# Kernel tuning notes

Hardware: AMD Instinct MI355X
Metric: run time of the kernel (lower is better)

Reference implementation:

```python
import jax, jax.numpy as jnp
import numpy as np

# Phi-3-small blocksparse config
S = 2048            # num prompt tokens (single sequence)
H = 32              # num query heads
HKV = 8             # num kv heads (GQA)
D = 128             # head size
BLK = 64            # sparse_block_size
LOCAL = 16          # local_blocks
VERT = 8            # vert_stride
SCALE = 0.08838834764831845  # 1/sqrt(128)
HEAD_SLIDE = max(1, VERT // H)  # = 1 (per-head vertical offset, homo_head=False)


def _blocksparse_mask():
    """Per-head local+strided block-sparse causal mask, shape [H, S, S] bool."""
    nb = S // BLK
    qb = jnp.arange(nb)[None, :, None]   # query block idx
    kb = jnp.arange(nb)[None, None, :]   # key block idx
    h = jnp.arange(H)[:, None, None]
    blk = (qb >= kb) & (
        (qb - kb < LOCAL) | (((kb + h * HEAD_SLIDE + 1) % VERT) == 0)
    )  # [H, nb, nb]
    dense = jnp.repeat(jnp.repeat(blk, BLK, axis=1), BLK, axis=2)  # [H, S, S]
    causal = jnp.arange(S)[:, None] >= jnp.arange(S)[None, :]
    return dense & causal[None]


def setup_inputs() -> dict:
    key = jax.random.key(0)
    k1, k2, k3 = jax.random.split(key, 3)
    return {
        "query": jax.random.normal(k1, (S, H * D), dtype=jnp.float32),
        "key": jax.random.normal(k2, (S, HKV * D), dtype=jnp.float32),
        "value": jax.random.normal(k3, (S, HKV * D), dtype=jnp.float32),
    }


def reference(query, key, value):
    q = query.reshape(S, H, D)
    k = jnp.repeat(key.reshape(S, HKV, D), H // HKV, axis=1)    # GQA expand
    v = jnp.repeat(value.reshape(S, HKV, D), H // HKV, axis=1)
    scores = jnp.einsum("qhd,khd->hqk", q, k) * SCALE           # [H, S, S]
    mask = _blocksparse_mask()
    scores = jnp.where(mask, scores, jnp.finfo(scores.dtype).min)
    p = jax.nn.softmax(scores, axis=-1)
    out = jnp.einsum("hqk,khd->qhd", p, v)                      # [S, H, D]
    return out.reshape(S, H * D)
```

## Files before the change

### kernel.cpp

```cpp
#include <hip/hip_runtime.h>


typedef __bf16 bf16_t;
typedef __bf16 bf16x4 __attribute__((ext_vector_type(4)));
typedef __bf16 bf16x8 __attribute__((ext_vector_type(8)));
typedef float  fx4    __attribute__((ext_vector_type(4)));
typedef unsigned u32x2 __attribute__((ext_vector_type(2)));
typedef unsigned u32x4 __attribute__((ext_vector_type(4)));

#define SL2E_F 0.1275240614354876f

__device__ inline void load_lds16(const bf16_t* g, bf16_t* l) {
    __builtin_amdgcn_global_load_lds(
        (const __attribute__((address_space(1))) void*)g,
        (__attribute__((address_space(3))) void*)l, 16, 0, 0);
}

__device__ inline unsigned cvt_pk_bf16(float lo, float hi) {
    unsigned r;
    asm("v_cvt_pk_bf16_f32 %0, %1, %2" : "=v"(r) : "v"(lo), "v"(hi));
    return r;
}

__device__ inline u32x2 quad_gather(unsigned A) {
    u32x2 bc = __builtin_amdgcn_permlane32_swap(A, A, false, false);
    return __builtin_amdgcn_permlane16_swap(bc[0], bc[1], false, false);
}

__global__ void prep_kernel(const float* __restrict__ K, const float* __restrict__ V,
                            bf16_t* __restrict__ Kb, bf16_t* __restrict__ VT)
{
    const int blk = blockIdx.x;
    {
        const size_t base = (size_t)blk * 4096 + (size_t)threadIdx.x * 16;
        fx4 a0 = *(const fx4*)(K + base);
        fx4 a1 = *(const fx4*)(K + base + 4);
        fx4 a2 = *(const fx4*)(K + base + 8);
        fx4 a3 = *(const fx4*)(K + base + 12);
        bf16x8 f0, f1;
        f0[0]=(bf16_t)a0[0]; f0[1]=(bf16_t)a0[1]; f0[2]=(bf16_t)a0[2]; f0[3]=(bf16_t)a0[3];
        f0[4]=(bf16_t)a1[0]; f0[5]=(bf16_t)a1[1]; f0[6]=(bf16_t)a1[2]; f0[7]=(bf16_t)a1[3];
        f1[0]=(bf16_t)a2[0]; f1[1]=(bf16_t)a2[1]; f1[2]=(bf16_t)a2[2]; f1[3]=(bf16_t)a2[3];
        f1[4]=(bf16_t)a3[0]; f1[5]=(bf16_t)a3[1]; f1[6]=(bf16_t)a3[2]; f1[7]=(bf16_t)a3[3];
        *(bf16x8*)(Kb + base)     = f0;
        *(bf16x8*)(Kb + base + 8) = f1;
    }
    __shared__ __align__(16) bf16_t T[64 * 72];
    const int s0 = (blk & 31) * 64;
    const int c0 = (blk >> 5) * 64;
    const int tx = threadIdx.x & 15, ty = threadIdx.x >> 4;
    fx4 a0 = *(const fx4*)(V + (size_t)(s0 + ty * 4 + 0) * 1024 + c0 + tx * 4);
    fx4 a1 = *(const fx4*)(V + (size_t)(s0 + ty * 4 + 1) * 1024 + c0 + tx * 4);
    fx4 a2 = *(const fx4*)(V + (size_t)(s0 + ty * 4 + 2) * 1024 + c0 + tx * 4);
    fx4 a3 = *(const fx4*)(V + (size_t)(s0 + ty * 4 + 3) * 1024 + c0 + tx * 4);
#pragma unroll
    for (int j = 0; j < 4; ++j) {
        bf16x4 f = { (bf16_t)a0[j], (bf16_t)a1[j], (bf16_t)a2[j], (bf16_t)a3[j] };
        *(bf16x4*)&T[(tx * 4 + j) * 72 + ty * 4] = f;
    }
    __syncthreads();
    const int c = threadIdx.x >> 2, part = threadIdx.x & 3;
    bf16x8 x0 = *(const bf16x8*)&T[c * 72 + part * 16];
    bf16x8 x1 = *(const bf16x8*)&T[c * 72 + part * 16 + 8];
    bf16_t* dst = VT + (size_t)(c0 + c) * 2048 + s0 + part * 16;
    *(bf16x8*)(dst)     = x0;
    *(bf16x8*)(dst + 8) = x1;
}

__launch_bounds__(128, 1)
__global__ void bsfa_kernel(const float* __restrict__ Q,
                            const bf16_t* __restrict__ Kb,
                            const bf16_t* __restrict__ VT,
                            float* __restrict__ O)
{
    const int blk  = blockIdx.x;
    const int kvh  = blk & 7;
    const int h    = kvh * 4 + ((blk >> 3) & 3);
    const int qb   = 31 - (blk >> 5);
    const int tid  = threadIdx.x;
    const int rh   = tid >> 6;
    const int lane = tid & 63;
    const int l15  = lane & 15;
    const int quad = lane >> 4;
    const bool hi32 = (lane >= 32);

    __shared__ __align__(16) bf16_t Ks[2][64 * 128];
    __shared__ __align__(16) bf16_t Vs[2][128 * 64];

    const int row0 = qb * 64 + rh * 32;

    const bf16_t* kg = Kb + (size_t)kvh * 128;
    const bf16_t* vg = VT + ((size_t)kvh * 128) * 2048;

    bf16x8 qf[2][4];
#pragma unroll
    for (int qt = 0; qt < 2; ++qt) {
        const float* qp = Q + (size_t)(row0 + qt * 16 + l15) * 4096 + h * 128;
#pragma unroll
        for (int kc = 0; kc < 4; ++kc) {
            fx4 a = *(const fx4*)(qp + kc * 32 + quad * 8);
            fx4 b = *(const fx4*)(qp + kc * 32 + quad * 8 + 4);
            bf16x8 f;
            f[0] = (bf16_t)(a[0] * SL2E_F); f[1] = (bf16_t)(a[1] * SL2E_F);
            f[2] = (bf16_t)(a[2] * SL2E_F); f[3] = (bf16_t)(a[3] * SL2E_F);
            f[4] = (bf16_t)(b[0] * SL2E_F); f[5] = (bf16_t)(b[1] * SL2E_F);
            f[6] = (bf16_t)(b[2] * SL2E_F); f[7] = (bf16_t)(b[3] * SL2E_F);
            qf[qt][kc] = f;
        }
    }

    bf16x8 ones;
#pragma unroll
    for (int i = 0; i < 8; ++i) ones[i] = (bf16_t)1.0f;

    fx4 oacc[8][2];
    fx4 lacc[2];
    const fx4 zero4 = {0.0f, 0.0f, 0.0f, 0.0f};
#pragma unroll
    for (int dt = 0; dt < 8; ++dt)
#pragma unroll
        for (int qt = 0; qt < 2; ++qt) oacc[dt][qt] = zero4;
    lacc[0] = zero4; lacc[1] = zero4;

    auto stage = [&](int kb, int bi) {
        const bf16_t* kt_g = kg + ((size_t)kb << 16);
        const bf16_t* vt_g = vg + ((size_t)kb << 6);
        bf16_t* kd = &Ks[bi][0];
        bf16_t* vd = &Vs[bi][0];
#pragma unroll
        for (int i = 0; i < 8; ++i) {
            const int chunk = i * 128 + tid;
            const int krow = chunk >> 4;
            const int kc   = (chunk & 15) ^ (krow & 15);
            load_lds16(kt_g + (size_t)krow * 1024 + kc * 8, kd + (size_t)chunk * 8);
            const int vrow = chunk >> 3;
            const int vc   = (chunk & 7) ^ (vrow & 7);
            load_lds16(vt_g + (size_t)vrow * 2048 + vc * 8, vd + (size_t)chunk * 8);
        }
    };

    const int loc0 = (qb > 15) ? (qb - 15) : 0;
    const int kb0s = (8 - ((h + 1) & 7)) & 7;
    auto nxt = [&](int kb) -> int {
        if (kb < loc0) { const int t = kb + 8; return (t <= qb - 16) ? t : loc0; }
        return (kb < qb) ? (kb + 1) : -1;
    };

    int kb = (qb - 16 >= kb0s) ? kb0s : loc0;
    stage(kb, 0);
    __syncthreads();

    int cur = 0;
    while (kb >= 0) {
        const int nkb = nxt(kb);
        if (nkb >= 0) stage(nkb, cur ^ 1);

        const bf16_t* kd = &Ks[cur][0];
        const bf16_t* vd = &Vs[cur][0];

        fx4 sacc[4][2];
#pragma unroll
        for (int kt = 0; kt < 4; ++kt)
#pragma unroll
            for (int qt = 0; qt < 2; ++qt) sacc[kt][qt] = zero4;
#pragma unroll
        for (int kc = 0; kc < 4; ++kc)
#pragma unroll
            for (int kt = 0; kt < 4; ++kt) {
                bf16x8 kf = *(const bf16x8*)&kd[(kt * 16 + l15) * 128 + ((kc * 4 + quad) ^ l15) * 8];
#pragma unroll
                for (int qt = 0; qt < 2; ++qt)
                    sacc[kt][qt] = __builtin_amdgcn_mfma_f32_16x16x32_bf16(
                        kf, qf[qt][kc], sacc[kt][qt], 0, 0, 0);
            }

        if (kb == qb) {
#pragma unroll
            for (int kt = 0; kt < 4; ++kt)
#pragma unroll
                for (int qt = 0; qt < 2; ++qt)
#pragma unroll
                    for (int r = 0; r < 4; ++r) {
                        const int k_in = kt * 16 + quad * 4 + r;
                        const int q_in = rh * 32 + qt * 16 + l15;
                        if (q_in < k_in) sacc[kt][qt][r] = -1e30f;
                    }
        }

#pragma unroll
        for (int kt = 0; kt < 4; ++kt)
#pragma unroll
            for (int qt = 0; qt < 2; ++qt)
#pragma unroll
                for (int r = 0; r < 4; ++r)
                    sacc[kt][qt][r] = exp2f(sacc[kt][qt][r]);

        bf16x8 pf[2][2];
#pragma unroll
        for (int qt = 0; qt < 2; ++qt)
#pragma unroll
            for (int kcg = 0; kcg < 2; ++kcg) {
                const unsigned a00 = cvt_pk_bf16(sacc[2*kcg  ][qt][0], sacc[2*kcg  ][qt][1]);
                const unsigned a01 = cvt_pk_bf16(sacc[2*kcg  ][qt][2], sacc[2*kcg  ][qt][3]);
                const unsigned a10 = cvt_pk_bf16(sacc[2*kcg+1][qt][0], sacc[2*kcg+1][qt][1]);
                const unsigned a11 = cvt_pk_bf16(sacc[2*kcg+1][qt][2], sacc[2*kcg+1][qt][3]);
                const u32x2 g00 = quad_gather(a00);
                const u32x2 g01 = quad_gather(a01);
                const u32x2 g10 = quad_gather(a10);
                const u32x2 g11 = quad_gather(a11);
                u32x4 pw;
                pw[0] = hi32 ? g10[0] : g00[0];
                pw[1] = hi32 ? g11[0] : g01[0];
                pw[2] = hi32 ? g10[1] : g00[1];
                pw[3] = hi32 ? g11[1] : g01[1];
                pf[qt][kcg] = __builtin_bit_cast(bf16x8, pw);
            }

#pragma unroll
        for (int kcg = 0; kcg < 2; ++kcg) {
#pragma unroll
            for (int dt = 0; dt < 8; ++dt) {
                bf16x8 vf = *(const bf16x8*)&vd[(dt * 16 + l15) * 64 + ((kcg * 4 + quad) ^ (l15 & 7)) * 8];
#pragma unroll
                for (int qt = 0; qt < 2; ++qt)
                    oacc[dt][qt] = __builtin_amdgcn_mfma_f32_16x16x32_bf16(
                        vf, pf[qt][kcg], oacc[dt][qt], 0, 0, 0);
            }
#pragma unroll
            for (int qt = 0; qt < 2; ++qt)
                lacc[qt] = __builtin_amdgcn_mfma_f32_16x16x32_bf16(
                    ones, pf[qt][kcg], lacc[qt], 0, 0, 0);
        }

        __syncthreads();
        kb = nkb; cur ^= 1;
    }

#pragma unroll
    for (int qt = 0; qt < 2; ++qt) {
        const float inv = 1.0f / lacc[qt][0];
#pragma unroll
        for (int dt = 0; dt < 8; ++dt) {
            fx4 o = oacc[dt][qt] * inv;
            *(fx4*)(O + (size_t)(row0 + qt * 16 + l15) * 4096 + h * 128 + dt * 16 + quad * 4) = o;
        }
    }
}

extern "C" void kernel_launch(void* const* d_in, const int* in_sizes, int n_in,
                              void* d_out, int out_size, void* d_ws, size_t ws_size,
                              hipStream_t stream) {
    (void)in_sizes; (void)n_in; (void)ws_size; (void)out_size;
    const float* q = (const float*)d_in[0];
    const float* k = (const float*)d_in[1];
    const float* v = (const float*)d_in[2];
    float* o = (float*)d_out;

    bf16_t* Kb = (bf16_t*)d_ws;
    bf16_t* VT = Kb + (size_t)2048 * 1024;

    prep_kernel<<<dim3(512), dim3(256), 0, stream>>>(k, v, Kb, VT);
    bsfa_kernel<<<dim3(1024), dim3(128), 0, stream>>>(q, Kb, VT, o);
}
```

Before: 164.6 us.

## Load V fragments directly from global memory into registers, drop V LDS staging

V tiles are no longer staged in shared memory through async global-to-LDS copies. Each lane now loads its V MFMA fragments straight from global memory into registers, issued early and spread around the QK^T MFMAs to hide latency. This halves LDS use, and launch bounds are raised to allow two blocks per CU. The cost is higher register pressure (16 extra bf16x8 per lane), uncoalesced-ish strided global loads of V, and redundant V reads by the two waves of a block.

```diff
diff --git a/kernel.cpp b/kernel.cpp
--- a/kernel.cpp
+++ b/kernel.cpp
@@ -67,7 +67,7 @@
     *(bf16x8*)(dst + 8) = x1;
 }
 
-__launch_bounds__(128, 1)
+__launch_bounds__(128, 2)
 __global__ void bsfa_kernel(const float* __restrict__ Q,
                             const bf16_t* __restrict__ Kb,
                             const bf16_t* __restrict__ VT,
@@ -85,12 +85,11 @@
     const bool hi32 = (lane >= 32);
 
     __shared__ __align__(16) bf16_t Ks[2][64 * 128];
-    __shared__ __align__(16) bf16_t Vs[2][128 * 64];
 
     const int row0 = qb * 64 + rh * 32;
 
     const bf16_t* kg = Kb + (size_t)kvh * 128;
-    const bf16_t* vg = VT + ((size_t)kvh * 128) * 2048;
+    const bf16_t* vbase = VT + ((size_t)kvh * 128 + l15) * 2048 + quad * 8;
 
     bf16x8 qf[2][4];
 #pragma unroll
@@ -124,18 +123,13 @@
 
     auto stage = [&](int kb, int bi) {
         const bf16_t* kt_g = kg + ((size_t)kb << 16);
-        const bf16_t* vt_g = vg + ((size_t)kb << 6);
         bf16_t* kd = &Ks[bi][0];
-        bf16_t* vd = &Vs[bi][0];
 #pragma unroll
         for (int i = 0; i < 8; ++i) {
             const int chunk = i * 128 + tid;
             const int krow = chunk >> 4;
             const int kc   = (chunk & 15) ^ (krow & 15);
             load_lds16(kt_g + (size_t)krow * 1024 + kc * 8, kd + (size_t)chunk * 8);
-            const int vrow = chunk >> 3;
-            const int vc   = (chunk & 7) ^ (vrow & 7);
-            load_lds16(vt_g + (size_t)vrow * 2048 + vc * 8, vd + (size_t)chunk * 8);
         }
     };
 
@@ -156,7 +150,12 @@
         if (nkb >= 0) stage(nkb, cur ^ 1);
 
         const bf16_t* kd = &Ks[cur][0];
-        const bf16_t* vd = &Vs[cur][0];
+        const bf16_t* vp = vbase + ((size_t)kb << 6);
+
+        bf16x8 vfr0[8];
+#pragma unroll
+        for (int dt = 0; dt < 8; ++dt)
+            vfr0[dt] = *(const bf16x8*)(vp + (size_t)(dt * 16) * 2048);
 
         fx4 sacc[4][2];
 #pragma unroll
@@ -173,6 +172,11 @@
                     sacc[kt][qt] = __builtin_amdgcn_mfma_f32_16x16x32_bf16(
                         kf, qf[qt][kc], sacc[kt][qt], 0, 0, 0);
             }
+
+        bf16x8 vfr1[8];
+#pragma unroll
+        for (int dt = 0; dt < 8; ++dt)
+            vfr1[dt] = *(const bf16x8*)(vp + (size_t)(dt * 16) * 2048 + 32);
 
         if (kb == qb) {
 #pragma unroll
@@ -217,20 +221,25 @@
             }
 
 #pragma unroll
-        for (int kcg = 0; kcg < 2; ++kcg) {
-#pragma unroll
-            for (int dt = 0; dt < 8; ++dt) {
-                bf16x8 vf = *(const bf16x8*)&vd[(dt * 16 + l15) * 64 + ((kcg * 4 + quad) ^ (l15 & 7)) * 8];
-#pragma unroll
-                for (int qt = 0; qt < 2; ++qt)
-                    oacc[dt][qt] = __builtin_amdgcn_mfma_f32_16x16x32_bf16(
-                        vf, pf[qt][kcg], oacc[dt][qt], 0, 0, 0);
-            }
+        for (int dt = 0; dt < 8; ++dt)
 #pragma unroll
             for (int qt = 0; qt < 2; ++qt)
-                lacc[qt] = __builtin_amdgcn_mfma_f32_16x16x32_bf16(
-                    ones, pf[qt][kcg], lacc[qt], 0, 0, 0);
-        }
+                oacc[dt][qt] = __builtin_amdgcn_mfma_f32_16x16x32_bf16(
+                    vfr0[dt], pf[qt][0], oacc[dt][qt], 0, 0, 0);
+#pragma unroll
+        for (int qt = 0; qt < 2; ++qt)
+            lacc[qt] = __builtin_amdgcn_mfma_f32_16x16x32_bf16(
+                ones, pf[qt][0], lacc[qt], 0, 0, 0);
+#pragma unroll
+        for (int dt = 0; dt < 8; ++dt)
+#pragma unroll
+            for (int qt = 0; qt < 2; ++qt)
+                oacc[dt][qt] = __builtin_amdgcn_mfma_f32_16x16x32_bf16(
+                    vfr1[dt], pf[qt][1], oacc[dt][qt], 0, 0, 0);
+#pragma unroll
+        for (int qt = 0; qt < 2; ++qt)
+            lacc[qt] = __builtin_amdgcn_mfma_f32_16x16x32_bf16(
+                ones, pf[qt][1], lacc[qt], 0, 0, 0);
 
         __syncthreads();
         kb = nkb; cur ^= 1;
```

Measured after the change: 162.2 us. About the same (-1.5%).
